# Kernel optimization log

Measured on AMD Instinct MI355X. Metric: run time of the kernel, lower is better.

## Reference

```python
import jax, jax.numpy as jnp
import numpy as np

D_IN = 1024
D_OUT = 1024
SEQ = 2048
BATCH = 4


def setup_inputs() -> dict:
    key = jax.random.key(0)
    k_x, k_q, k_k, k_v = jax.random.split(key, 4)
    scale = 1.0 / np.sqrt(D_IN)  # ~ torch Linear init scale
    x = jax.random.normal(k_x, (BATCH, SEQ, D_IN), dtype=jnp.float32)
    # torch nn.Linear weights have shape [d_out, d_in]; y = x @ W.T
    Wq = jax.random.uniform(k_q, (D_OUT, D_IN), jnp.float32, -scale, scale)
    Wk = jax.random.uniform(k_k, (D_OUT, D_IN), jnp.float32, -scale, scale)
    Wv = jax.random.uniform(k_v, (D_OUT, D_IN), jnp.float32, -scale, scale)
    return {"x": x, "Wq": Wq, "Wk": Wk, "Wv": Wv}


def reference(x, Wq, Wk, Wv):
    # projections (no bias, qkv_bias=False)
    q = jnp.einsum("bsd,ed->bse", x, Wq)  # [B,S,D_OUT]
    k = jnp.einsum("bsd,ed->bse", x, Wk)
    v = jnp.einsum("bsd,ed->bse", x, Wv)
    scores = jnp.einsum("bqe,bke->bqk", q, k)  # [B,S,S]
    seq = scores.shape[-1]
    causal = jnp.tril(jnp.ones((seq, seq), dtype=bool))  # keep lower-tri
    scores = jnp.where(causal[None], scores, -jnp.inf)
    # note: original scales AFTER masking: softmax(scores / sqrt(d_k))
    inv_sqrt_dk = 1.0 / np.sqrt(k.shape[-1]).astype(np.float32)
    weights = jax.nn.softmax(scores * inv_sqrt_dk, axis=-1)
    # dropout p=0.0 (eval-equivalent): identity
    return jnp.einsum("bqk,bke->bqe", weights, v)
```

## Files before the change

### kernel.cpp

```cpp
#include <hip/hip_runtime.h>
#include <hip/hip_bf16.h>

typedef __bf16 v8bf __attribute__((ext_vector_type(8)));
typedef float v4f __attribute__((ext_vector_type(4)));

#define GBL_AS(p) ((const __attribute__((address_space(1))) unsigned int*)(p))
#define LDS_AS(p) ((__attribute__((address_space(3))) unsigned int*)(p))

#define WAIT_VM3() __builtin_amdgcn_s_waitcnt(0x0F73)
#define WAIT_VM4() __builtin_amdgcn_s_waitcnt(0x0F74)
#define WAIT_VM0() __builtin_amdgcn_s_waitcnt(0x0F70)

__global__ void cast_f32_bf16(const float* __restrict__ src,
                              __hip_bfloat16* __restrict__ dst, int n) {
  int i = (blockIdx.x * 256 + threadIdx.x) * 4;
  if (i >= n) return;
  float4 f = *(const float4*)(src + i);
  union { __hip_bfloat16 h[4]; uint2 u; } pk;
  pk.h[0] = __float2bfloat16(f.x);
  pk.h[1] = __float2bfloat16(f.y);
  pk.h[2] = __float2bfloat16(f.z);
  pk.h[3] = __float2bfloat16(f.w);
  *(uint2*)(dst + i) = pk.u;
}

__global__ void cast_w3(const float* __restrict__ a, const float* __restrict__ b,
                        const float* __restrict__ c, __hip_bfloat16* __restrict__ dst) {
  int seg = blockIdx.x >> 10;
  const float* src = seg == 0 ? a : (seg == 1 ? b : c);
  int i = ((blockIdx.x & 1023) * 256 + threadIdx.x) * 4;
  float4 f = *(const float4*)(src + i);
  union { __hip_bfloat16 h[4]; uint2 u; } pk;
  pk.h[0] = __float2bfloat16(f.x);
  pk.h[1] = __float2bfloat16(f.y);
  pk.h[2] = __float2bfloat16(f.z);
  pk.h[3] = __float2bfloat16(f.w);
  *(uint2*)(dst + seg * 1048576 + i) = pk.u;
}

__global__ __launch_bounds__(256, 2)
void gemm_proj(const __hip_bfloat16* __restrict__ A, int lda,
               const __hip_bfloat16* __restrict__ B, long sBb, int ldb,
               __hip_bfloat16* __restrict__ C, long sCb, int ldc,
               float scale, __hip_bfloat16* __restrict__ vTp) {
  const int tid = threadIdx.x;
  const int l = tid & 63, w = tid >> 6;
  const int z  = blockIdx.x >> 3;
  const int nb = (blockIdx.x & 7) << 7;
  const int mb = blockIdx.y << 8;

  B += (long)z * sBb;

  __shared__ alignas(16) __hip_bfloat16 As[3][256 * 32];
  __shared__ alignas(16) __hip_bfloat16 Bs[3][128 * 32];

  v4f acc[8][4] = {};
  const int wm = (w >> 1) << 7;
  const int wn = (w & 1) << 6;

  const int qa0 = 0 * 256 + w * 64 + l, ra0 = qa0 >> 2;
  const int qa1 = 1 * 256 + w * 64 + l, ra1 = qa1 >> 2;
  const int qa2 = 2 * 256 + w * 64 + l, ra2 = qa2 >> 2;
  const int qa3 = 3 * 256 + w * 64 + l, ra3 = qa3 >> 2;
  const __hip_bfloat16* sA0 = A + (long)(mb + ra0) * lda + (((qa0 & 3) ^ ((ra0 >> 1) & 3)) << 3);
  const __hip_bfloat16* sA1 = A + (long)(mb + ra1) * lda + (((qa1 & 3) ^ ((ra1 >> 1) & 3)) << 3);
  const __hip_bfloat16* sA2 = A + (long)(mb + ra2) * lda + (((qa2 & 3) ^ ((ra2 >> 1) & 3)) << 3);
  const __hip_bfloat16* sA3 = A + (long)(mb + ra3) * lda + (((qa3 & 3) ^ ((ra3 >> 1) & 3)) << 3);
  const int qb0 = 0 * 256 + w * 64 + l, rb0 = qb0 >> 2;
  const int qb1 = 1 * 256 + w * 64 + l, rb1 = qb1 >> 2;
  const __hip_bfloat16* sB0 = B + (long)(nb + rb0) * ldb + (((qb0 & 3) ^ ((rb0 >> 1) & 3)) << 3);
  const __hip_bfloat16* sB1 = B + (long)(nb + rb1) * ldb + (((qb1 & 3) ^ ((rb1 >> 1) & 3)) << 3);

  const int arow = wm + (l & 15);
  const int ldsA = arow * 32 + ((((l >> 4) ^ ((arow >> 1) & 3))) << 3);
  const int brow = wn + (l & 15);
  const int ldsB = brow * 32 + ((((l >> 4) ^ ((brow >> 1) & 3))) << 3);

#define STAGE_P(K0, BUF) do {                                                   \
    __builtin_amdgcn_global_load_lds(GBL_AS(sA0 + (K0)),                        \
        LDS_AS(&As[BUF][0 * 2048 + w * 512]), 16, 0, 0);                        \
    __builtin_amdgcn_global_load_lds(GBL_AS(sA1 + (K0)),                        \
        LDS_AS(&As[BUF][1 * 2048 + w * 512]), 16, 0, 0);                        \
    __builtin_amdgcn_global_load_lds(GBL_AS(sA2 + (K0)),                        \
        LDS_AS(&As[BUF][2 * 2048 + w * 512]), 16, 0, 0);                        \
    __builtin_amdgcn_global_load_lds(GBL_AS(sA3 + (K0)),                        \
        LDS_AS(&As[BUF][3 * 2048 + w * 512]), 16, 0, 0);                        \
    __builtin_amdgcn_global_load_lds(GBL_AS(sB0 + (K0)),                        \
        LDS_AS(&Bs[BUF][0 * 2048 + w * 512]), 16, 0, 0);                        \
    __builtin_amdgcn_global_load_lds(GBL_AS(sB1 + (K0)),                        \
        LDS_AS(&Bs[BUF][1 * 2048 + w * 512]), 16, 0, 0);                        \
  } while (0)

#define COMPUTE_P(BI) do {                                                      \
    v8bf af[8], bfr[4];                                                         \
    _Pragma("unroll")                                                           \
    for (int i = 0; i < 8; ++i)                                                 \
      af[i]  = *(const v8bf*)(&As[BI][ldsA + i * 512]);                         \
    _Pragma("unroll")                                                           \
    for (int j = 0; j < 4; ++j)                                                 \
      bfr[j] = *(const v8bf*)(&Bs[BI][ldsB + j * 512]);                         \
    _Pragma("unroll")                                                           \
    for (int i = 0; i < 8; ++i)                                                 \
      _Pragma("unroll")                                                         \
      for (int j = 0; j < 4; ++j)                                               \
        acc[i][j] = __builtin_amdgcn_mfma_f32_16x16x32_bf16(af[i], bfr[j],      \
                                                            acc[i][j], 0, 0, 0);\
  } while (0)

#define WAIT_VM6_() __builtin_amdgcn_s_waitcnt(0x0F76)
#define KITER_P(IT) do {                                                        \
    if constexpr ((IT) < 31) WAIT_VM6_(); else WAIT_VM0();                      \
    __builtin_amdgcn_s_barrier();                                               \
    if constexpr ((IT) < 30) STAGE_P((IT) * 32 + 64, ((IT) + 2) % 3);           \
    COMPUTE_P((IT) % 3);                                                        \
  } while (0)

  STAGE_P(0, 0);
  STAGE_P(32, 1);
  KITER_P(0);  KITER_P(1);  KITER_P(2);  KITER_P(3);  KITER_P(4);  KITER_P(5);
  KITER_P(6);  KITER_P(7);  KITER_P(8);  KITER_P(9);  KITER_P(10); KITER_P(11);
  KITER_P(12); KITER_P(13); KITER_P(14); KITER_P(15); KITER_P(16); KITER_P(17);
  KITER_P(18); KITER_P(19); KITER_P(20); KITER_P(21); KITER_P(22); KITER_P(23);
  KITER_P(24); KITER_P(25); KITER_P(26); KITER_P(27); KITER_P(28); KITER_P(29);
  KITER_P(30); KITER_P(31);
#undef KITER_P
#undef COMPUTE_P
#undef STAGE_P

  const int col0 = nb + wn + (l & 15);
  const int row0 = mb + wm + ((l >> 4) << 2);
  if (z < 2) {
    __hip_bfloat16* Cz = C + (long)z * sCb;
#pragma unroll
    for (int i = 0; i < 8; ++i)
#pragma unroll
      for (int r = 0; r < 4; ++r) {
        long ro = (long)(row0 + i * 16 + r) * ldc;
#pragma unroll
        for (int j = 0; j < 4; ++j)
          Cz[ro + col0 + j * 16] = __float2bfloat16(acc[i][j][r] * scale);
      }
  } else {
    const long b = row0 >> 11;
    const int seq0 = row0 & 2047;
#pragma unroll
    for (int i = 0; i < 8; ++i)
#pragma unroll
      for (int j = 0; j < 4; ++j) {
        union { __hip_bfloat16 h[4]; uint2 u; } pk;
#pragma unroll
        for (int r = 0; r < 4; ++r) pk.h[r] = __float2bfloat16(acc[i][j][r]);
        *(uint2*)(vTp + b * 2097152 + (long)(col0 + j * 16) * 2048 +
                  (seq0 + i * 16)) = pk.u;
      }
  }
}

__global__ __launch_bounds__(256, 4)
void gemm_score64(const __hip_bfloat16* __restrict__ A, long sAb,
                  const __hip_bfloat16* __restrict__ B, long sBb,
                  __hip_bfloat16* __restrict__ C, long sCb,
                  float scale, float* __restrict__ sums) {
  const int tid = threadIdx.x;
  const int l = tid & 63, w = tid >> 6;
  const int id = blockIdx.x;
  const int z = id / 272;
  const int t = id - z * 272;
  int p = (int)((__builtin_sqrtf(4.0f * t + 1.0f) - 1.0f) * 0.5f);
  while ((p + 1) * (p + 2) <= t) ++p;
  while (p * (p + 1) > t) --p;
  const int rem = t - p * (p + 1);
  const int mm = 2 * p + (rem > p);
  const int nn = (rem > p) ? rem - (p + 1) : rem;
  const int mb = mm << 6, nb = nn << 7;

  const __hip_bfloat16* Az = A + (long)z * sAb;
  const __hip_bfloat16* Bz = B + (long)z * sBb;

  __shared__ alignas(16) __hip_bfloat16 As[3][64 * 32];
  __shared__ alignas(16) __hip_bfloat16 Bs[3][128 * 32];

  v4f acc[4][2] = {};
  const int wn = w << 5;

  const int ras = tid >> 2;
  const int cas = ((tid & 3) ^ ((ras >> 1) & 3)) << 3;
  const __hip_bfloat16* Arow = Az + (long)(mb + ras) * 1024 + cas;
  const int r0s = tid >> 2;
  const int c0s = ((tid & 3) ^ ((r0s >> 1) & 3)) << 3;
  const int q1 = 256 + tid, r1s = q1 >> 2;
  const int c1s = ((q1 & 3) ^ ((r1s >> 1) & 3)) << 3;
  const __hip_bfloat16* Brow0 = Bz + (long)(nb + r0s) * 1024 + c0s;
  const __hip_bfloat16* Brow1 = Bz + (long)(nb + r1s) * 1024 + c1s;

  const int arow = l & 15;
  const int ldsA = arow * 32 + ((((l >> 4) ^ ((arow >> 1) & 3))) << 3);
  const int brow = wn + (l & 15);
  const int ldsB = brow * 32 + ((((l >> 4) ^ ((brow >> 1) & 3))) << 3);

#define STAGE_S(K0, BUF) do {                                                   \
    __builtin_amdgcn_global_load_lds(GBL_AS(Arow + (K0)),                       \
        LDS_AS(&As[BUF][tid * 8]), 16, 0, 0);                                   \
    __builtin_amdgcn_global_load_lds(GBL_AS(Brow0 + (K0)),                      \
        LDS_AS(&Bs[BUF][tid * 8]), 16, 0, 0);                                   \
    __builtin_amdgcn_global_load_lds(GBL_AS(Brow1 + (K0)),                      \
        LDS_AS(&Bs[BUF][2048 + tid * 8]), 16, 0, 0);                            \
  } while (0)

#define COMPUTE_S(BI) do {                                                      \
    v8bf af[4], bfr[2];                                                         \
    _Pragma("unroll")                                                           \
    for (int i = 0; i < 4; ++i)                                                 \
      af[i]  = *(const v8bf*)(&As[BI][ldsA + i * 512]);                         \
    _Pragma("unroll")                                                           \
    for (int j = 0; j < 2; ++j)                                                 \
      bfr[j] = *(const v8bf*)(&Bs[BI][ldsB + j * 512]);                         \
    _Pragma("unroll")                                                           \
    for (int i = 0; i < 4; ++i)                                                 \
      _Pragma("unroll")                                                         \
      for (int j = 0; j < 2; ++j)                                               \
        acc[i][j] = __builtin_amdgcn_mfma_f32_16x16x32_bf16(af[i], bfr[j],      \
                                                            acc[i][j], 0, 0, 0);\
  } while (0)

#define KITER_S(IT) do {                                                        \
    if constexpr ((IT) < 31) WAIT_VM3(); else WAIT_VM0();                       \
    __builtin_amdgcn_s_barrier();                                               \
    if constexpr ((IT) < 30) STAGE_S((IT) * 32 + 64, ((IT) + 2) % 3);           \
    COMPUTE_S((IT) % 3);                                                        \
  } while (0)

  STAGE_S(0, 0);
  STAGE_S(32, 1);
  KITER_S(0);  KITER_S(1);  KITER_S(2);  KITER_S(3);  KITER_S(4);  KITER_S(5);
  KITER_S(6);  KITER_S(7);  KITER_S(8);  KITER_S(9);  KITER_S(10); KITER_S(11);
  KITER_S(12); KITER_S(13); KITER_S(14); KITER_S(15); KITER_S(16); KITER_S(17);
  KITER_S(18); KITER_S(19); KITER_S(20); KITER_S(21); KITER_S(22); KITER_S(23);
  KITER_S(24); KITER_S(25); KITER_S(26); KITER_S(27); KITER_S(28); KITER_S(29);
  KITER_S(30); KITER_S(31);
#undef KITER_S
#undef COMPUTE_S
#undef STAGE_S

  __hip_bfloat16* Cz = C + (long)z * sCb;
  float* srow = sums + z * 2048;
  const int col0 = nb + wn + (l & 15);
  const int row0 = mb + ((l >> 4) << 2);
#pragma unroll
  for (int i = 0; i < 4; ++i)
#pragma unroll
    for (int r = 0; r < 4; ++r) {
      const int m = row0 + i * 16 + r;
      const long ro = (long)m * 2048;
      float sp = 0.f;
#pragma unroll
      for (int j = 0; j < 2; ++j) {
        const int n = col0 + j * 16;
        float pv = (n <= m) ? __expf(acc[i][j][r] * scale) : 0.0f;
        sp += pv;
        Cz[ro + n] = __float2bfloat16(pv);
      }
      sp += __shfl_xor(sp, 1);
      sp += __shfl_xor(sp, 2);
      sp += __shfl_xor(sp, 4);
      sp += __shfl_xor(sp, 8);
      if ((l & 15) == 0) atomicAdd(&srow[m], sp);
    }
}

__global__ __launch_bounds__(256, 3)
void gemm_pv(const __hip_bfloat16* __restrict__ A, long sAb, int lda,
             const __hip_bfloat16* __restrict__ B, long sBb, int ldb,
             float* __restrict__ C, long sCb, int ldc,
             const float* __restrict__ sums) {
  const int tid = threadIdx.x;
  const int l = tid & 63, w = tid >> 6;
  const int id = blockIdx.x;
  const int z = id / 192;
  const int rem = id - z * 192;
  const int nn = rem / 24, s = rem - nn * 24;
  int m, k0s, klen;
  bool atom;
  if (s < 8) {
    m = s; k0s = 0; klen = (m + 1) << 7; atom = false;
  } else {
    const int u = s - 8;
    m = 8 + (u >> 1);
    const int h = ((m + 1) >> 1) << 7;
    if (u & 1) { k0s = h; klen = ((m + 1) << 7) - h; }
    else       { k0s = 0; klen = h; }
    atom = true;
  }
  const int mb = m << 7, nb = nn << 7;

  A += (long)z * sAb + k0s;
  B += (long)z * sBb + k0s;

  __shared__ alignas(16) __hip_bfloat16 As[3][128 * 32];
  __shared__ alignas(16) __hip_bfloat16 Bs[3][128 * 32];

  v4f acc[4][4] = {};
  const int wm = (w >> 1) * 64, wn = (w & 1) * 64;

  const int cb0 = w * 64;
  const int q0 = cb0 + l, r0s = q0 >> 2;
  const int c0s = ((q0 & 3) ^ ((r0s >> 1) & 3)) << 3;
  const int cb1 = 256 + w * 64;
  const int q1 = cb1 + l, r1s = q1 >> 2;
  const int c1s = ((q1 & 3) ^ ((r1s >> 1) & 3)) << 3;

  const __hip_bfloat16* Arow0 = A + (long)(mb + r0s) * lda + c0s;
  const __hip_bfloat16* Arow1 = A + (long)(mb + r1s) * lda + c1s;
  const __hip_bfloat16* Brow0 = B + (long)(nb + r0s) * ldb + c0s;
  const __hip_bfloat16* Brow1 = B + (long)(nb + r1s) * ldb + c1s;

  const int arow = wm + (l & 15);
  const int ldsA = arow * 32 + ((((l >> 4) ^ ((arow >> 1) & 3))) << 3);
  const int brow = wn + (l & 15);
  const int ldsB = brow * 32 + ((((l >> 4) ^ ((brow >> 1) & 3))) << 3);

  auto stage = [&](int k0, int buf) {
    __builtin_amdgcn_global_load_lds(GBL_AS(Arow0 + k0),
        LDS_AS(&As[buf][cb0 * 8]), 16, 0, 0);
    __builtin_amdgcn_global_load_lds(GBL_AS(Brow0 + k0),
        LDS_AS(&Bs[buf][cb0 * 8]), 16, 0, 0);
    __builtin_amdgcn_global_load_lds(GBL_AS(Arow1 + k0),
        LDS_AS(&As[buf][cb1 * 8]), 16, 0, 0);
    __builtin_amdgcn_global_load_lds(GBL_AS(Brow1 + k0),
        LDS_AS(&Bs[buf][cb1 * 8]), 16, 0, 0);
  };
  stage(0, 0);
  if (32 < klen) stage(32, 1);
  int bi = 0;
  for (int k0 = 0; k0 < klen; k0 += 32) {
    if (k0 + 32 < klen) WAIT_VM4(); else WAIT_VM0();
    __builtin_amdgcn_s_barrier();
    if (k0 + 64 < klen) stage(k0 + 64, bi == 0 ? 2 : bi - 1);
    v8bf af[4], bfr[4];
#pragma unroll
    for (int i = 0; i < 4; ++i) {
      af[i]  = *(const v8bf*)(&As[bi][ldsA + i * 512]);
      bfr[i] = *(const v8bf*)(&Bs[bi][ldsB + i * 512]);
    }
#pragma unroll
    for (int i = 0; i < 4; ++i)
#pragma unroll
      for (int j = 0; j < 4; ++j)
        acc[i][j] = __builtin_amdgcn_mfma_f32_16x16x32_bf16(af[i], bfr[j], acc[i][j], 0, 0, 0);
    bi = (bi == 2) ? 0 : bi + 1;
  }

  float* Cz = C + (long)z * sCb;
  const float* srow = sums + z * 2048;
  const int col0 = nb + wn + (l & 15);
  const int row0 = mb + wm + ((l >> 4) << 2);
#pragma unroll
  for (int i = 0; i < 4; ++i)
#pragma unroll
    for (int r = 0; r < 4; ++r) {
      const int mr = row0 + i * 16 + r;
      const float sc = 1.0f / srow[mr];
      const long ro = (long)mr * ldc;
#pragma unroll
      for (int j = 0; j < 4; ++j) {
        const float v = acc[i][j][r] * sc;
        if (atom) atomicAdd(&Cz[ro + col0 + j * 16], v);
        else Cz[ro + col0 + j * 16] = v;
      }
    }
}

extern "C" void kernel_launch(void* const* d_in, const int* in_sizes, int n_in,
                              void* d_out, int out_size, void* d_ws, size_t ws_size,
                              hipStream_t stream) {
  const float* x  = (const float*)d_in[0];
  const float* Wq = (const float*)d_in[1];
  const float* Wk = (const float*)d_in[2];
  const float* Wv = (const float*)d_in[3];
  float* out = (float*)d_out;
  char* ws = (char*)d_ws;

  __hip_bfloat16* qkv = (__hip_bfloat16*)ws;
  __hip_bfloat16* vT  = (__hip_bfloat16*)(ws + 50331648);
  __hip_bfloat16* xb  = (__hip_bfloat16*)(ws + 67108864);
  __hip_bfloat16* Wb  = (__hip_bfloat16*)(ws + 83886080);
  __hip_bfloat16* P   = (__hip_bfloat16*)(ws + 67108864);
  float* sums         = (float*)(ws + 100663296);

  hipMemsetAsync(sums, 0, 8192 * sizeof(float), stream);
  for (int z = 0; z < 4; ++z)
    hipMemsetAsync(out + (long)z * 2097152 + 1048576, 0, 4194304, stream);

  cast_f32_bf16<<<8192, 256, 0, stream>>>(x, xb, 8388608);
  cast_w3<<<3072, 256, 0, stream>>>(Wq, Wk, Wv, Wb);

  gemm_proj<<<dim3(24, 32, 1), 256, 0, stream>>>(
      xb, 1024, Wb, 1048576L, 1024, qkv, 8388608L, 1024, 1.0f, vT);

  gemm_score64<<<dim3(1088, 1, 1), 256, 0, stream>>>(
      qkv, 2097152L, qkv + 8388608, 2097152L,
      P, 4194304L, 0.03125f, sums);

  gemm_pv<<<dim3(768, 1, 1), 256, 0, stream>>>(
      P, 4194304L, 2048, vT, 2097152L, 2048,
      out, 2097152L, 1024, sums);
}
```

Measured before the change: 267.1 us.

## Use 128x128 score tiles and drop split-K atomics in PV GEMM

```diff
diff --git a/kernel.cpp b/kernel.cpp
--- a/kernel.cpp
+++ b/kernel.cpp
@@ -7,8 +7,8 @@
 #define GBL_AS(p) ((const __attribute__((address_space(1))) unsigned int*)(p))
 #define LDS_AS(p) ((__attribute__((address_space(3))) unsigned int*)(p))
 
-#define WAIT_VM3() __builtin_amdgcn_s_waitcnt(0x0F73)
 #define WAIT_VM4() __builtin_amdgcn_s_waitcnt(0x0F74)
+#define WAIT_VM6() __builtin_amdgcn_s_waitcnt(0x0F76)
 #define WAIT_VM0() __builtin_amdgcn_s_waitcnt(0x0F70)
 
 __global__ void cast_f32_bf16(const float* __restrict__ src,
@@ -107,9 +107,8 @@
                                                             acc[i][j], 0, 0, 0);\
   } while (0)
 
-#define WAIT_VM6_() __builtin_amdgcn_s_waitcnt(0x0F76)
 #define KITER_P(IT) do {                                                        \
-    if constexpr ((IT) < 31) WAIT_VM6_(); else WAIT_VM0();                      \
+    if constexpr ((IT) < 31) WAIT_VM6(); else WAIT_VM0();                       \
     __builtin_amdgcn_s_barrier();                                               \
     if constexpr ((IT) < 30) STAGE_P((IT) * 32 + 64, ((IT) + 2) % 3);           \
     COMPUTE_P((IT) % 3);                                                        \
@@ -156,75 +155,77 @@
   }
 }
 
-__global__ __launch_bounds__(256, 4)
-void gemm_score64(const __hip_bfloat16* __restrict__ A, long sAb,
-                  const __hip_bfloat16* __restrict__ B, long sBb,
-                  __hip_bfloat16* __restrict__ C, long sCb,
-                  float scale, float* __restrict__ sums) {
+__global__ __launch_bounds__(256, 3)
+void gemm_score(const __hip_bfloat16* __restrict__ A, long sAb,
+                const __hip_bfloat16* __restrict__ B, long sBb,
+                __hip_bfloat16* __restrict__ C, long sCb,
+                float scale, float* __restrict__ sums) {
   const int tid = threadIdx.x;
   const int l = tid & 63, w = tid >> 6;
   const int id = blockIdx.x;
-  const int z = id / 272;
-  const int t = id - z * 272;
-  int p = (int)((__builtin_sqrtf(4.0f * t + 1.0f) - 1.0f) * 0.5f);
-  while ((p + 1) * (p + 2) <= t) ++p;
-  while (p * (p + 1) > t) --p;
-  const int rem = t - p * (p + 1);
-  const int mm = 2 * p + (rem > p);
-  const int nn = (rem > p) ? rem - (p + 1) : rem;
-  const int mb = mm << 6, nb = nn << 7;
+  const int wk = (id & 7) * 68 + (id >> 3);
+  const int z = wk / 136;
+  const int t = wk - z * 136;
+  int m = (int)((__builtin_sqrtf(8.0f * t + 1.0f) - 1.0f) * 0.5f);
+  while ((m + 1) * (m + 2) / 2 <= t) ++m;
+  while (m * (m + 1) / 2 > t) --m;
+  const int mb = m << 7;
+  const int nb = (t - m * (m + 1) / 2) << 7;
 
   const __hip_bfloat16* Az = A + (long)z * sAb;
   const __hip_bfloat16* Bz = B + (long)z * sBb;
 
-  __shared__ alignas(16) __hip_bfloat16 As[3][64 * 32];
+  __shared__ alignas(16) __hip_bfloat16 As[3][128 * 32];
   __shared__ alignas(16) __hip_bfloat16 Bs[3][128 * 32];
 
-  v4f acc[4][2] = {};
-  const int wn = w << 5;
-
-  const int ras = tid >> 2;
-  const int cas = ((tid & 3) ^ ((ras >> 1) & 3)) << 3;
-  const __hip_bfloat16* Arow = Az + (long)(mb + ras) * 1024 + cas;
-  const int r0s = tid >> 2;
-  const int c0s = ((tid & 3) ^ ((r0s >> 1) & 3)) << 3;
-  const int q1 = 256 + tid, r1s = q1 >> 2;
+  v4f acc[4][4] = {};
+  const int wm = (w >> 1) * 64, wn = (w & 1) * 64;
+
+  const int cb0 = w * 64;
+  const int q0 = cb0 + l, r0s = q0 >> 2;
+  const int c0s = ((q0 & 3) ^ ((r0s >> 1) & 3)) << 3;
+  const int cb1 = 256 + w * 64;
+  const int q1 = cb1 + l, r1s = q1 >> 2;
   const int c1s = ((q1 & 3) ^ ((r1s >> 1) & 3)) << 3;
+
+  const __hip_bfloat16* Arow0 = Az + (long)(mb + r0s) * 1024 + c0s;
+  const __hip_bfloat16* Arow1 = Az + (long)(mb + r1s) * 1024 + c1s;
   const __hip_bfloat16* Brow0 = Bz + (long)(nb + r0s) * 1024 + c0s;
   const __hip_bfloat16* Brow1 = Bz + (long)(nb + r1s) * 1024 + c1s;
 
-  const int arow = l & 15;
+  const int arow = wm + (l & 15);
   const int ldsA = arow * 32 + ((((l >> 4) ^ ((arow >> 1) & 3))) << 3);
   const int brow = wn + (l & 15);
   const int ldsB = brow * 32 + ((((l >> 4) ^ ((brow >> 1) & 3))) << 3);
 
 #define STAGE_S(K0, BUF) do {                                                   \
-    __builtin_amdgcn_global_load_lds(GBL_AS(Arow + (K0)),                       \
-        LDS_AS(&As[BUF][tid * 8]), 16, 0, 0);                                   \
+    __builtin_amdgcn_global_load_lds(GBL_AS(Arow0 + (K0)),                      \
+        LDS_AS(&As[BUF][cb0 * 8]), 16, 0, 0);                                   \
     __builtin_amdgcn_global_load_lds(GBL_AS(Brow0 + (K0)),                      \
-        LDS_AS(&Bs[BUF][tid * 8]), 16, 0, 0);                                   \
+        LDS_AS(&Bs[BUF][cb0 * 8]), 16, 0, 0);                                   \
+    __builtin_amdgcn_global_load_lds(GBL_AS(Arow1 + (K0)),                      \
+        LDS_AS(&As[BUF][cb1 * 8]), 16, 0, 0);                                   \
     __builtin_amdgcn_global_load_lds(GBL_AS(Brow1 + (K0)),                      \
-        LDS_AS(&Bs[BUF][2048 + tid * 8]), 16, 0, 0);                            \
+        LDS_AS(&Bs[BUF][cb1 * 8]), 16, 0, 0);                                   \
   } while (0)
 
 #define COMPUTE_S(BI) do {                                                      \
-    v8bf af[4], bfr[2];                                                         \
-    _Pragma("unroll")                                                           \
-    for (int i = 0; i < 4; ++i)                                                 \
+    v8bf af[4], bfr[4];                                                         \
+    _Pragma("unroll")                                                           \
+    for (int i = 0; i < 4; ++i) {                                               \
       af[i]  = *(const v8bf*)(&As[BI][ldsA + i * 512]);                         \
-    _Pragma("unroll")                                                           \
-    for (int j = 0; j < 2; ++j)                                                 \
-      bfr[j] = *(const v8bf*)(&Bs[BI][ldsB + j * 512]);                         \
+      bfr[i] = *(const v8bf*)(&Bs[BI][ldsB + i * 512]);                         \
+    }                                                                           \
     _Pragma("unroll")                                                           \
     for (int i = 0; i < 4; ++i)                                                 \
       _Pragma("unroll")                                                         \
-      for (int j = 0; j < 2; ++j)                                               \
+      for (int j = 0; j < 4; ++j)                                               \
         acc[i][j] = __builtin_amdgcn_mfma_f32_16x16x32_bf16(af[i], bfr[j],      \
                                                             acc[i][j], 0, 0, 0);\
   } while (0)
 
 #define KITER_S(IT) do {                                                        \
-    if constexpr ((IT) < 31) WAIT_VM3(); else WAIT_VM0();                       \
+    if constexpr ((IT) < 31) WAIT_VM4(); else WAIT_VM0();                       \
     __builtin_amdgcn_s_barrier();                                               \
     if constexpr ((IT) < 30) STAGE_S((IT) * 32 + 64, ((IT) + 2) % 3);           \
     COMPUTE_S((IT) % 3);                                                        \
@@ -245,18 +246,18 @@
   __hip_bfloat16* Cz = C + (long)z * sCb;
   float* srow = sums + z * 2048;
   const int col0 = nb + wn + (l & 15);
-  const int row0 = mb + ((l >> 4) << 2);
+  const int row0 = mb + wm + ((l >> 4) << 2);
 #pragma unroll
   for (int i = 0; i < 4; ++i)
 #pragma unroll
     for (int r = 0; r < 4; ++r) {
-      const int m = row0 + i * 16 + r;
-      const long ro = (long)m * 2048;
+      const int mm = row0 + i * 16 + r;
+      const long ro = (long)mm * 2048;
       float sp = 0.f;
 #pragma unroll
-      for (int j = 0; j < 2; ++j) {
+      for (int j = 0; j < 4; ++j) {
         const int n = col0 + j * 16;
-        float pv = (n <= m) ? __expf(acc[i][j][r] * scale) : 0.0f;
+        float pv = (n <= mm) ? __expf(acc[i][j][r] * scale) : 0.0f;
         sp += pv;
         Cz[ro + n] = __float2bfloat16(pv);
       }
@@ -264,7 +265,7 @@
       sp += __shfl_xor(sp, 2);
       sp += __shfl_xor(sp, 4);
       sp += __shfl_xor(sp, 8);
-      if ((l & 15) == 0) atomicAdd(&srow[m], sp);
+      if ((l & 15) == 0) atomicAdd(&srow[mm], sp);
     }
 }
 
@@ -276,25 +277,15 @@
   const int tid = threadIdx.x;
   const int l = tid & 63, w = tid >> 6;
   const int id = blockIdx.x;
-  const int z = id / 192;
-  const int rem = id - z * 192;
-  const int nn = rem / 24, s = rem - nn * 24;
-  int m, k0s, klen;
-  bool atom;
-  if (s < 8) {
-    m = s; k0s = 0; klen = (m + 1) << 7; atom = false;
-  } else {
-    const int u = s - 8;
-    m = 8 + (u >> 1);
-    const int h = ((m + 1) >> 1) << 7;
-    if (u & 1) { k0s = h; klen = ((m + 1) << 7) - h; }
-    else       { k0s = 0; klen = h; }
-    atom = true;
-  }
-  const int mb = m << 7, nb = nn << 7;
-
-  A += (long)z * sAb + k0s;
-  B += (long)z * sBb + k0s;
+  const int x = id & 7, j = id >> 3;
+  const int z = x >> 1;
+  const int nb = (((x & 1) << 2) | (j & 3)) << 7;
+  const int m = 15 - (j >> 2);
+  const int mb = m << 7;
+  const int kend = (m + 1) << 7;
+
+  A += (long)z * sAb;
+  B += (long)z * sBb;
 
   __shared__ alignas(16) __hip_bfloat16 As[3][128 * 32];
   __shared__ alignas(16) __hip_bfloat16 Bs[3][128 * 32];
@@ -330,12 +321,12 @@
         LDS_AS(&Bs[buf][cb1 * 8]), 16, 0, 0);
   };
   stage(0, 0);
-  if (32 < klen) stage(32, 1);
+  if (32 < kend) stage(32, 1);
   int bi = 0;
-  for (int k0 = 0; k0 < klen; k0 += 32) {
-    if (k0 + 32 < klen) WAIT_VM4(); else WAIT_VM0();
+  for (int k0 = 0; k0 < kend; k0 += 32) {
+    if (k0 + 32 < kend) WAIT_VM4(); else WAIT_VM0();
     __builtin_amdgcn_s_barrier();
-    if (k0 + 64 < klen) stage(k0 + 64, bi == 0 ? 2 : bi - 1);
+    if (k0 + 64 < kend) stage(k0 + 64, bi == 0 ? 2 : bi - 1);
     v8bf af[4], bfr[4];
 #pragma unroll
     for (int i = 0; i < 4; ++i) {
@@ -345,8 +336,8 @@
 #pragma unroll
     for (int i = 0; i < 4; ++i)
 #pragma unroll
-      for (int j = 0; j < 4; ++j)
-        acc[i][j] = __builtin_amdgcn_mfma_f32_16x16x32_bf16(af[i], bfr[j], acc[i][j], 0, 0, 0);
+      for (int jj = 0; jj < 4; ++jj)
+        acc[i][jj] = __builtin_amdgcn_mfma_f32_16x16x32_bf16(af[i], bfr[jj], acc[i][jj], 0, 0, 0);
     bi = (bi == 2) ? 0 : bi + 1;
   }
 
@@ -362,11 +353,8 @@
       const float sc = 1.0f / srow[mr];
       const long ro = (long)mr * ldc;
 #pragma unroll
-      for (int j = 0; j < 4; ++j) {
-        const float v = acc[i][j][r] * sc;
-        if (atom) atomicAdd(&Cz[ro + col0 + j * 16], v);
-        else Cz[ro + col0 + j * 16] = v;
-      }
+      for (int jj = 0; jj < 4; ++jj)
+        Cz[ro + col0 + jj * 16] = acc[i][jj][r] * sc;
     }
 }
 
@@ -388,8 +376,6 @@
   float* sums         = (float*)(ws + 100663296);
 
   hipMemsetAsync(sums, 0, 8192 * sizeof(float), stream);
-  for (int z = 0; z < 4; ++z)
-    hipMemsetAsync(out + (long)z * 2097152 + 1048576, 0, 4194304, stream);
 
   cast_f32_bf16<<<8192, 256, 0, stream>>>(x, xb, 8388608);
   cast_w3<<<3072, 256, 0, stream>>>(Wq, Wk, Wv, Wb);
@@ -397,11 +383,11 @@
   gemm_proj<<<dim3(24, 32, 1), 256, 0, stream>>>(
       xb, 1024, Wb, 1048576L, 1024, qkv, 8388608L, 1024, 1.0f, vT);
 
-  gemm_score64<<<dim3(1088, 1, 1), 256, 0, stream>>>(
+  gemm_score<<<dim3(544, 1, 1), 256, 0, stream>>>(
       qkv, 2097152L, qkv + 8388608, 2097152L,
       P, 4194304L, 0.03125f, sums);
 
-  gemm_pv<<<dim3(768, 1, 1), 256, 0, stream>>>(
+  gemm_pv<<<dim3(512, 1, 1), 256, 0, stream>>>(
       P, 4194304L, 2048, vT, 2097152L, 2048,
       out, 2097152L, 1024, sums);
 }
```

After: 230.8 us. -13.6%, faster.
